# Kernel tuning notes

Hardware: AMD Instinct MI355X
Metric: run time of the kernel (lower is better)

## Reference

```python
import jax, jax.numpy as jnp
import numpy as np

B, S, HID = 1, 2048, 4096
H, HKV, D = 32, 8, 128
GROUPS = H // HKV
ROPE_BASE = 10000.0


def setup_inputs() -> dict:
    key = jax.random.key(0)
    k1, k2, k3, k4, k5 = jax.random.split(key, 5)
    s = 0.02
    return {
        "hidden_states": jax.random.normal(k1, (B, S, HID), dtype=jnp.float32),
        "Wq": jax.random.normal(k2, (H * D, HID), dtype=jnp.float32) * s,
        "Wk": jax.random.normal(k3, (HKV * D, HID), dtype=jnp.float32) * s,
        "Wv": jax.random.normal(k4, (HKV * D, HID), dtype=jnp.float32) * s,
        "Wo": jax.random.normal(k5, (HID, H * D), dtype=jnp.float32) * s,
    }


def _rotate_half(x):
    x1, x2 = x[..., : D // 2], x[..., D // 2 :]
    return jnp.concatenate((-x2, x1), axis=-1)


def _rope_tables(seq_len):
    inv_freq = 1.0 / (ROPE_BASE ** (jnp.arange(0, D, 2, dtype=jnp.float32) / D))
    t = jnp.arange(seq_len, dtype=jnp.float32)
    freqs = jnp.outer(t, inv_freq)            # [S, D/2]
    emb = jnp.concatenate((freqs, freqs), -1)  # [S, D]
    return jnp.cos(emb)[None, None], jnp.sin(emb)[None, None]  # [1,1,S,D]


def reference(hidden_states, Wq, Wk, Wv, Wo):
    b, s, _ = hidden_states.shape
    scale = D ** -0.5
    q = (hidden_states @ Wq.T).reshape(b, s, H, D).transpose(0, 2, 1, 3)    # [B,H,S,D]
    k = (hidden_states @ Wk.T).reshape(b, s, HKV, D).transpose(0, 2, 1, 3)  # [B,HKV,S,D]
    v = (hidden_states @ Wv.T).reshape(b, s, HKV, D).transpose(0, 2, 1, 3)

    cos, sin = _rope_tables(s)
    q = q * cos + _rotate_half(q) * sin
    k = k * cos + _rotate_half(k) * sin

    # repeat_kv: h = kv_h * groups + g -> consecutive repeat along head axis
    k_rep = jnp.repeat(k, GROUPS, axis=1)  # [B,H,S,D]
    v_rep = jnp.repeat(v, GROUPS, axis=1)

    scores = jnp.einsum("bhqd,bhkd->bhqk", q, k_rep) * scale
    causal = jnp.tril(jnp.ones((s, s), dtype=bool))
    scores = jnp.where(causal[None, None], scores, jnp.finfo(scores.dtype).min)
    probs = jax.nn.softmax(scores, axis=-1)
    attn = jnp.einsum("bhqk,bhkd->bhqd", probs, v_rep)  # [B,H,S,D]
    attn = attn.transpose(0, 2, 1, 3).reshape(b, s, H * D)
    return attn @ Wo.T
```

## Files before the change

kernel.cpp:

```cpp
#include <hip/hip_runtime.h>

#define AS1 __attribute__((address_space(1)))
#define AS3 __attribute__((address_space(3)))

typedef __bf16 bf16;
typedef __bf16 bf16x8 __attribute__((ext_vector_type(8)));
typedef float f32x4 __attribute__((ext_vector_type(4)));

__device__ __forceinline__ void gld_lds16(const bf16* g, bf16* l) {
    __builtin_amdgcn_global_load_lds((const AS1 void*)g, (AS3 void*)l, 16, 0, 0);
}

__global__ void cvt4_kernel(const float4* __restrict__ in, ushort4* __restrict__ out, int n4) {
    const int i = blockIdx.x * 256 + threadIdx.x;
    if (i >= n4) return;
    const float4 v = in[i];
    ushort4 r;
    r.x = __builtin_bit_cast(unsigned short, (bf16)v.x);
    r.y = __builtin_bit_cast(unsigned short, (bf16)v.y);
    r.z = __builtin_bit_cast(unsigned short, (bf16)v.z);
    r.w = __builtin_bit_cast(unsigned short, (bf16)v.w);
    out[i] = r;
}

template <int BN, bool OUTF32>
__launch_bounds__(512, 2)
__global__ void gemm8p_kernel(const bf16* __restrict__ A, const bf16* __restrict__ W,
                              void* __restrict__ Cout, int M, int N, int K) {
    constexpr int NF = BN / 64;
    constexpr int IB = BN / 128;
    __shared__ __align__(16) bf16 Asl[4][128 * 32];
    __shared__ __align__(16) bf16 Bsl[4][BN * 32];

    const int tn = blockIdx.x * BN;
    const int tm = blockIdx.y * 128;
    const int tid = threadIdx.x;
    const int wave = tid >> 6;
    const int lane = tid & 63;
    const int laneR = lane & 15;
    const int laneS = lane >> 4;
    const int wmB = (wave >> 2) * 64;
    const int wnB = (wave & 3) * (BN / 4);
    const int NT = K >> 5;

    auto stage = [&](int t) {
        const int slot = t & 3;
        const int k0 = t << 5;
        {
            const int row = tid >> 2, g = tid & 3;
            gld_lds16(A + (size_t)(tm + row) * K + k0 + g * 8, &Asl[slot][wave * 512]);
        }
#pragma unroll
        for (int i = 0; i < IB; ++i) {
            const int row = i * 128 + (tid >> 2), g = tid & 3;
            gld_lds16(W + (size_t)(tn + row) * K + k0 + g * 8,
                      &Bsl[slot][i * 4096 + wave * 512]);
        }
    };

    f32x4 acc[4][NF] = {};

    stage(0); stage(1); stage(2);
    if constexpr (BN == 384) asm volatile("s_waitcnt vmcnt(8)" ::: "memory");
    else                     asm volatile("s_waitcnt vmcnt(6)" ::: "memory");
    __builtin_amdgcn_sched_barrier(0);
    __builtin_amdgcn_s_barrier();
    __builtin_amdgcn_sched_barrier(0);

    for (int t = 0; t < NT; ++t) {
        const int slot = t & 3;
        bf16x8 af[4], bfr[NF];
#pragma unroll
        for (int mf = 0; mf < 4; ++mf)
            af[mf] = *(const bf16x8*)&Asl[slot][(wmB + mf * 16 + laneR) * 32 + laneS * 8];
#pragma unroll
        for (int nf = 0; nf < NF; ++nf)
            bfr[nf] = *(const bf16x8*)&Bsl[slot][(wnB + nf * 16 + laneR) * 32 + laneS * 8];

        if (t + 3 < NT) stage(t + 3);

#pragma unroll
        for (int mf = 0; mf < 4; ++mf)
#pragma unroll
            for (int nf = 0; nf < NF; ++nf)
                acc[mf][nf] = __builtin_amdgcn_mfma_f32_16x16x32_bf16(af[mf], bfr[nf], acc[mf][nf], 0, 0, 0);

        __builtin_amdgcn_sched_barrier(0);
        if (t + 3 < NT) {
            if constexpr (BN == 384) asm volatile("s_waitcnt vmcnt(8)" ::: "memory");
            else                     asm volatile("s_waitcnt vmcnt(6)" ::: "memory");
        } else if (t + 3 == NT) {
            if constexpr (BN == 384) asm volatile("s_waitcnt vmcnt(4)" ::: "memory");
            else                     asm volatile("s_waitcnt vmcnt(3)" ::: "memory");
        } else {
            asm volatile("s_waitcnt vmcnt(0)" ::: "memory");
        }
        __builtin_amdgcn_sched_barrier(0);
        __builtin_amdgcn_s_barrier();
        __builtin_amdgcn_sched_barrier(0);
    }

    const int rbase = laneS * 4;
#pragma unroll
    for (int mf = 0; mf < 4; ++mf)
#pragma unroll
        for (int nf = 0; nf < NF; ++nf)
#pragma unroll
            for (int rr = 0; rr < 4; ++rr) {
                const size_t row = (size_t)tm + wmB + mf * 16 + rbase + rr;
                const size_t col = (size_t)tn + wnB + nf * 16 + laneR;
                if constexpr (OUTF32) ((float*)Cout)[row * N + col] = acc[mf][nf][rr];
                else                  ((bf16*)Cout)[row * N + col] = (bf16)acc[mf][nf][rr];
            }
    (void)M;
}

__global__ void rope_qk_kernel(const bf16* __restrict__ C, bf16* __restrict__ Qr, bf16* __restrict__ Kr) {
    const int idx = blockIdx.x * 256 + threadIdx.x;
    const int NQ = 2048 * 32 * 64;
    const float QSC = 0.12751743561884394f;
    const float LN1E4_64 = 0.14391156831212787f;
    if (idx < NQ) {
        const int f = idx & 63;
        const int t = idx >> 6;
        const int h = t & 31;
        const int s = t >> 5;
        const float x1 = (float)C[(size_t)s * 6144 + h * 128 + f];
        const float x2 = (float)C[(size_t)s * 6144 + h * 128 + f + 64];
        const float th = s * expf(-LN1E4_64 * (float)f);
        const float cs = cosf(th), sn = sinf(th);
        bf16* dst = Qr + ((size_t)h * 2048 + s) * 128 + f;
        dst[0]  = (bf16)((x1 * cs - x2 * sn) * QSC);
        dst[64] = (bf16)((x2 * cs + x1 * sn) * QSC);
    } else {
        const int i2 = idx - NQ;
        const int f = i2 & 63;
        const int t = i2 >> 6;
        const int h = t & 7;
        const int s = t >> 3;
        const float x1 = (float)C[(size_t)s * 6144 + 4096 + h * 128 + f];
        const float x2 = (float)C[(size_t)s * 6144 + 4096 + h * 128 + f + 64];
        const float th = s * expf(-LN1E4_64 * (float)f);
        const float cs = cosf(th), sn = sinf(th);
        bf16* dst = Kr + ((size_t)h * 2048 + s) * 128 + f;
        dst[0]  = (bf16)(x1 * cs - x2 * sn);
        dst[64] = (bf16)(x2 * cs + x1 * sn);
    }
}

__global__ void transpose_v_kernel(const bf16* __restrict__ C, bf16* __restrict__ Vt) {
    __shared__ __align__(16) unsigned short t[64][136];
    const int hkv = blockIdx.x >> 5;
    const int st = blockIdx.x & 31;
    const int s0 = st * 64;
    const int tid = threadIdx.x;
#pragma unroll
    for (int it = 0; it < 4; ++it) {
        const int l = it * 2048 + tid * 8;
        const int r = l >> 7, c = l & 127;
        *(bf16x8*)&t[r][c] = *(const bf16x8*)&C[(size_t)(s0 + r) * 6144 + 5120 + hkv * 128 + c];
    }
    __syncthreads();
#pragma unroll
    for (int it = 0; it < 8; ++it) {
        const int o = it * 1024 + tid * 4;
        const int d = o >> 6, j = o & 63;
        ushort4 pk;
        pk.x = t[j + 0][d];
        pk.y = t[j + 1][d];
        pk.z = t[j + 2][d];
        pk.w = t[j + 3][d];
        *(ushort4*)&Vt[((size_t)hkv * 128 + d) * 2048 + s0 + j] = pk;
    }
}

__launch_bounds__(256, 1)
__global__ void flash_attn_kernel(const bf16* __restrict__ Qr, const bf16* __restrict__ Kr,
                                  const bf16* __restrict__ Vt, bf16* __restrict__ Aout) {
    __shared__ __align__(16) bf16 Klds[2][128 * 128];
    __shared__ __align__(16) bf16 Vlds[2][128 * 128];
    __shared__ __align__(16) char Plds[4][4096];

    const int bid = blockIdx.x;
    const int hkv = bid & 7;
    const int r = bid >> 3;
    const int h = hkv * 4 + (r & 3);
    const int pa = r >> 2;
    const int qbA = 15 - pa, qbB = pa;
    const int tid = threadIdx.x;
    const int wave = tid >> 6, lane = tid & 63;
    const int laneR = lane & 15;
    const int laneS = lane >> 4;
    const int laneK = laneS * 8;
    const int rbase = laneS * 4;

    const bf16* Kh = Kr + (size_t)hkv * 2048 * 128;
    const bf16* Vh = Vt + (size_t)hkv * 128 * 2048;
    char* Pw = Plds[wave];

    auto stageK = [&](int kv0, int buf) {
#pragma unroll
        for (int s = 0; s < 8; ++s) {
            const int chunk = wave * 8 + s;
            const int L = chunk * 64 + lane;
            const int row = L >> 4, sl = L & 15;
            gld_lds16(Kh + (size_t)(kv0 + row) * 128 + ((sl ^ (row & 7)) << 3),
                      &Klds[buf][chunk * 512]);
        }
    };
    auto stageV = [&](int kv0, int buf) {
#pragma unroll
        for (int s = 0; s < 8; ++s) {
            const int chunk = wave * 8 + s;
            const int L = chunk * 64 + lane;
            const int row = L >> 4, sl = L & 15;
            gld_lds16(Vh + (size_t)row * 2048 + kv0 + ((sl ^ (row & 7)) << 3),
                      &Vlds[buf][chunk * 512]);
        }
    };

    int qbcur = qbA;
    int q0w = qbA * 128 + wave * 32;
    int tloc = 0;

    bf16x8 qf[2][4];
    auto loadQ = [&]() {
#pragma unroll
        for (int mi = 0; mi < 2; ++mi)
#pragma unroll
            for (int kc = 0; kc < 4; ++kc)
                qf[mi][kc] = *(const bf16x8*)&Qr[((size_t)h * 2048 + q0w + mi * 16 + laneR) * 128 + kc * 32 + laneK];
    };
    loadQ();

    f32x4 o[2][8] = {};
    float mrow[2][4], lrow[2][4];
#pragma unroll
    for (int mi = 0; mi < 2; ++mi)
#pragma unroll
        for (int rr = 0; rr < 4; ++rr) { mrow[mi][rr] = -1e30f; lrow[mi][rr] = 0.f; }

    stageK(0, 0);
    stageV(0, 0);
    __syncthreads();

    for (int g = 0; g < 17; ++g) {
        const int buf = g & 1;
        if (g < 16) {
            const int tn = (g + 1 <= qbA) ? (g + 1) : (g - qbA);
            stageK(tn * 128, buf ^ 1);
            stageV(tn * 128, buf ^ 1);
        }
        const int kv0 = tloc * 128;

        f32x4 sc[2][8] = {};
        __builtin_amdgcn_s_setprio(1);
#pragma unroll
        for (int kc = 0; kc < 4; ++kc) {
            bf16x8 kf[8];
#pragma unroll
            for (int j = 0; j < 8; ++j) {
                const int row = j * 16 + laneR;
                kf[j] = *(const bf16x8*)((const char*)Klds[buf] + row * 256 +
                                         ((kc * 64 + laneS * 16) ^ ((row & 7) << 4)));
            }
#pragma unroll
            for (int mi = 0; mi < 2; ++mi)
#pragma unroll
                for (int j = 0; j < 8; ++j)
                    sc[mi][j] = __builtin_amdgcn_mfma_f32_16x16x32_bf16(qf[mi][kc], kf[j], sc[mi][j], 0, 0, 0);
        }
        __builtin_amdgcn_s_setprio(0);

        if (tloc == qbcur) {
#pragma unroll
            for (int mi = 0; mi < 2; ++mi)
#pragma unroll
                for (int j = 0; j < 8; ++j)
#pragma unroll
                    for (int rr = 0; rr < 4; ++rr) {
                        const int qr = q0w + mi * 16 + rbase + rr;
                        const int kr = kv0 + j * 16 + laneR;
                        if (kr > qr) sc[mi][j][rr] = -1e30f;
                    }
        }

#pragma unroll
        for (int mi = 0; mi < 2; ++mi) {
#pragma unroll
            for (int rr = 0; rr < 4; ++rr) {
                float v = sc[mi][0][rr];
#pragma unroll
                for (int j = 1; j < 8; ++j) v = fmaxf(v, sc[mi][j][rr]);
                v = fmaxf(v, __shfl_xor(v, 1, 64));
                v = fmaxf(v, __shfl_xor(v, 2, 64));
                v = fmaxf(v, __shfl_xor(v, 4, 64));
                v = fmaxf(v, __shfl_xor(v, 8, 64));
                float m0 = mrow[mi][rr];
                if (v - m0 > 8.0f) {
                    const float fac = __builtin_exp2f(m0 - v);
                    mrow[mi][rr] = v;
                    m0 = v;
                    lrow[mi][rr] *= fac;
#pragma unroll
                    for (int j = 0; j < 8; ++j) o[mi][j][rr] *= fac;
                }
                float rs = 0.f;
#pragma unroll
                for (int j = 0; j < 8; ++j) {
                    const float p = __builtin_exp2f(sc[mi][j][rr] - m0);
                    sc[mi][j][rr] = p;
                    rs += p;
                }
                rs += __shfl_xor(rs, 1, 64);
                rs += __shfl_xor(rs, 2, 64);
                rs += __shfl_xor(rs, 4, 64);
                rs += __shfl_xor(rs, 8, 64);
                lrow[mi][rr] += rs;
            }
        }

#pragma unroll
        for (int hf = 0; hf < 2; ++hf) {
#pragma unroll
            for (int mi = 0; mi < 2; ++mi)
#pragma unroll
                for (int j = 0; j < 4; ++j)
#pragma unroll
                    for (int rr = 0; rr < 4; ++rr) {
                        const int row = mi * 16 + rbase + rr;
                        *(bf16*)(Pw + row * 128 + ((j * 32 + laneR * 2) ^ ((row & 7) << 4))) =
                            (bf16)sc[mi][hf * 4 + j][rr];
                    }
            __builtin_amdgcn_s_setprio(1);
#pragma unroll
            for (int kc = 0; kc < 2; ++kc) {
                bf16x8 pf[2];
#pragma unroll
                for (int mi = 0; mi < 2; ++mi) {
                    const int row = mi * 16 + laneR;
                    pf[mi] = *(const bf16x8*)(Pw + row * 128 + ((kc * 64 + laneS * 16) ^ ((row & 7) << 4)));
                }
                const int kcg = hf * 2 + kc;
                bf16x8 vf[8];
#pragma unroll
                for (int j = 0; j < 8; ++j) {
                    const int row = j * 16 + laneR;
                    vf[j] = *(const bf16x8*)((const char*)Vlds[buf] + row * 256 +
                                             ((kcg * 64 + laneS * 16) ^ ((row & 7) << 4)));
                }
#pragma unroll
                for (int mi = 0; mi < 2; ++mi)
#pragma unroll
                    for (int j = 0; j < 8; ++j)
                        o[mi][j] = __builtin_amdgcn_mfma_f32_16x16x32_bf16(pf[mi], vf[j], o[mi][j], 0, 0, 0);
            }
            __builtin_amdgcn_s_setprio(0);
        }

        if (tloc == qbcur) {
#pragma unroll
            for (int mi = 0; mi < 2; ++mi) {
                float rinv[4];
#pragma unroll
                for (int rr = 0; rr < 4; ++rr) rinv[rr] = 1.0f / lrow[mi][rr];
#pragma unroll
                for (int j = 0; j < 8; ++j)
#pragma unroll
                    for (int rr = 0; rr < 4; ++rr) {
                        const size_t row = (size_t)q0w + mi * 16 + rbase + rr;
                        Aout[row * 4096 + h * 128 + j * 16 + laneR] = (bf16)(o[mi][j][rr] * rinv[rr]);
                    }
            }
            if (g < 16) {
                qbcur = qbB;
                q0w = qbB * 128 + wave * 32;
                tloc = 0;
                loadQ();
#pragma unroll
                for (int mi = 0; mi < 2; ++mi)
#pragma unroll
                    for (int rr = 0; rr < 4; ++rr) { mrow[mi][rr] = -1e30f; lrow[mi][rr] = 0.f; }
#pragma unroll
                for (int mi = 0; mi < 2; ++mi)
#pragma unroll
                    for (int j = 0; j < 8; ++j)
                        o[mi][j] = f32x4{0.f, 0.f, 0.f, 0.f};
            }
        } else {
            ++tloc;
        }

        __syncthreads();
    }
}

extern "C" void kernel_launch(void* const* d_in, const int* in_sizes, int n_in,
                              void* d_out, int out_size, void* d_ws, size_t ws_size,
                              hipStream_t stream) {
    const float* hidden = (const float*)d_in[0];
    const float* Wq = (const float*)d_in[1];
    const float* Wk = (const float*)d_in[2];
    const float* Wv = (const float*)d_in[3];
    const float* Wo = (const float*)d_in[4];
    float* out = (float*)d_out;
    char* ws = (char*)d_ws;

    bf16* hs = (bf16*)(ws + 0);
    bf16* Wb = (bf16*)(ws + 16777216);
    bf16* Cq = (bf16*)(ws + 100663296);
    bf16* Qr = (bf16*)(ws + 125829120);
    bf16* Kr = (bf16*)(ws + 142606336);
    bf16* Vt = (bf16*)(ws + 146800640);
    bf16* At = (bf16*)(ws + 150994944);
    (void)ws_size; (void)in_sizes; (void)n_in; (void)out_size;

    cvt4_kernel<<<8192, 256, 0, stream>>>((const float4*)hidden, (ushort4*)hs, 2097152);
    cvt4_kernel<<<16384, 256, 0, stream>>>((const float4*)Wq, (ushort4*)(Wb + 0), 4194304);
    cvt4_kernel<<<4096, 256, 0, stream>>>((const float4*)Wk, (ushort4*)(Wb + 16777216), 1048576);
    cvt4_kernel<<<4096, 256, 0, stream>>>((const float4*)Wv, (ushort4*)(Wb + 20971520), 1048576);
    cvt4_kernel<<<16384, 256, 0, stream>>>((const float4*)Wo, (ushort4*)(Wb + 25165824), 4194304);

    gemm8p_kernel<384, false><<<dim3(16, 16), 512, 0, stream>>>(hs, Wb, Cq, 2048, 6144, 4096);

    rope_qk_kernel<<<20480, 256, 0, stream>>>(Cq, Qr, Kr);

    transpose_v_kernel<<<256, 256, 0, stream>>>(Cq, Vt);

    flash_attn_kernel<<<256, 256, 0, stream>>>(Qr, Kr, Vt, At);

    gemm8p_kernel<256, true><<<dim3(16, 16), 512, 0, stream>>>(At, Wb + 25165824, out, 2048, 4096, 4096);
}
```

Measured before the change: 353.0 us.

## Replace GEMM with 4-wave 128x256 tile kernel using swizzled LDS ring

Replaces the 8-wave, 4-slot GEMM with a 256-thread kernel. Each wave owns a 128x64 output slice, and the kernel uses a 3-slot LDS ring with prefetch distance 2. LDS is XOR-swizzled to avoid bank conflicts on the fragment reads, and the MFMA block is wrapped in s_setprio. This gives each wave more MFMA work per LDS read and fixes the tile shape at 128x256 for both projections, which changes the QKV grid to 24x16. The trade-offs are higher register pressure from 32 accumulators per wave and a shallower prefetch pipeline.

```diff
diff --git a/kernel.cpp b/kernel.cpp
--- a/kernel.cpp
+++ b/kernel.cpp
@@ -23,78 +23,76 @@
     out[i] = r;
 }
 
-template <int BN, bool OUTF32>
-__launch_bounds__(512, 2)
-__global__ void gemm8p_kernel(const bf16* __restrict__ A, const bf16* __restrict__ W,
-                              void* __restrict__ Cout, int M, int N, int K) {
-    constexpr int NF = BN / 64;
-    constexpr int IB = BN / 128;
-    __shared__ __align__(16) bf16 Asl[4][128 * 32];
-    __shared__ __align__(16) bf16 Bsl[4][BN * 32];
-
-    const int tn = blockIdx.x * BN;
+template <bool OUTF32>
+__launch_bounds__(256, 2)
+__global__ void gemm_ring_kernel(const bf16* __restrict__ A, const bf16* __restrict__ W,
+                                 void* __restrict__ Cout, int M, int N, int K) {
+    __shared__ __align__(16) bf16 Asl[3][128 * 32];
+    __shared__ __align__(16) bf16 Bsl[3][256 * 32];
+
+    const int tn = blockIdx.x * 256;
     const int tm = blockIdx.y * 128;
     const int tid = threadIdx.x;
     const int wave = tid >> 6;
     const int lane = tid & 63;
     const int laneR = lane & 15;
     const int laneS = lane >> 4;
-    const int wmB = (wave >> 2) * 64;
-    const int wnB = (wave & 3) * (BN / 4);
+    const int wnB = wave * 64;
     const int NT = K >> 5;
+    const int sofs = (laneS ^ ((laneR >> 1) & 3)) << 3;
 
     auto stage = [&](int t) {
-        const int slot = t & 3;
+        const int slot = t % 3;
         const int k0 = t << 5;
-        {
-            const int row = tid >> 2, g = tid & 3;
-            gld_lds16(A + (size_t)(tm + row) * K + k0 + g * 8, &Asl[slot][wave * 512]);
-        }
-#pragma unroll
-        for (int i = 0; i < IB; ++i) {
-            const int row = i * 128 + (tid >> 2), g = tid & 3;
-            gld_lds16(W + (size_t)(tn + row) * K + k0 + g * 8,
-                      &Bsl[slot][i * 4096 + wave * 512]);
+#pragma unroll
+        for (int iss = 0; iss < 2; ++iss) {
+            const int c = iss * 256 + wave * 64 + lane;
+            const int row = c >> 2;
+            const int sg = (c & 3) ^ ((row >> 1) & 3);
+            gld_lds16(A + (size_t)(tm + row) * K + k0 + sg * 8,
+                      &Asl[slot][iss * 2048 + wave * 512]);
+        }
+#pragma unroll
+        for (int iss = 0; iss < 4; ++iss) {
+            const int c = iss * 256 + wave * 64 + lane;
+            const int row = c >> 2;
+            const int sg = (c & 3) ^ ((row >> 1) & 3);
+            gld_lds16(W + (size_t)(tn + row) * K + k0 + sg * 8,
+                      &Bsl[slot][iss * 2048 + wave * 512]);
         }
     };
 
-    f32x4 acc[4][NF] = {};
-
-    stage(0); stage(1); stage(2);
-    if constexpr (BN == 384) asm volatile("s_waitcnt vmcnt(8)" ::: "memory");
-    else                     asm volatile("s_waitcnt vmcnt(6)" ::: "memory");
+    f32x4 acc[8][4] = {};
+
+    stage(0); stage(1);
+    asm volatile("s_waitcnt vmcnt(6)" ::: "memory");
     __builtin_amdgcn_sched_barrier(0);
     __builtin_amdgcn_s_barrier();
     __builtin_amdgcn_sched_barrier(0);
 
     for (int t = 0; t < NT; ++t) {
-        const int slot = t & 3;
-        bf16x8 af[4], bfr[NF];
-#pragma unroll
-        for (int mf = 0; mf < 4; ++mf)
-            af[mf] = *(const bf16x8*)&Asl[slot][(wmB + mf * 16 + laneR) * 32 + laneS * 8];
-#pragma unroll
-        for (int nf = 0; nf < NF; ++nf)
-            bfr[nf] = *(const bf16x8*)&Bsl[slot][(wnB + nf * 16 + laneR) * 32 + laneS * 8];
-
-        if (t + 3 < NT) stage(t + 3);
-
-#pragma unroll
-        for (int mf = 0; mf < 4; ++mf)
-#pragma unroll
-            for (int nf = 0; nf < NF; ++nf)
+        const int slot = t % 3;
+        if (t + 2 < NT) stage(t + 2);
+
+        bf16x8 af[8], bfr[4];
+#pragma unroll
+        for (int nf = 0; nf < 4; ++nf)
+            bfr[nf] = *(const bf16x8*)&Bsl[slot][(wnB + nf * 16 + laneR) * 32 + sofs];
+#pragma unroll
+        for (int mf = 0; mf < 8; ++mf)
+            af[mf] = *(const bf16x8*)&Asl[slot][(mf * 16 + laneR) * 32 + sofs];
+
+        __builtin_amdgcn_s_setprio(1);
+#pragma unroll
+        for (int mf = 0; mf < 8; ++mf)
+#pragma unroll
+            for (int nf = 0; nf < 4; ++nf)
                 acc[mf][nf] = __builtin_amdgcn_mfma_f32_16x16x32_bf16(af[mf], bfr[nf], acc[mf][nf], 0, 0, 0);
+        __builtin_amdgcn_s_setprio(0);
 
         __builtin_amdgcn_sched_barrier(0);
-        if (t + 3 < NT) {
-            if constexpr (BN == 384) asm volatile("s_waitcnt vmcnt(8)" ::: "memory");
-            else                     asm volatile("s_waitcnt vmcnt(6)" ::: "memory");
-        } else if (t + 3 == NT) {
-            if constexpr (BN == 384) asm volatile("s_waitcnt vmcnt(4)" ::: "memory");
-            else                     asm volatile("s_waitcnt vmcnt(3)" ::: "memory");
-        } else {
-            asm volatile("s_waitcnt vmcnt(0)" ::: "memory");
-        }
+        if (t + 2 < NT) asm volatile("s_waitcnt vmcnt(6)" ::: "memory");
+        else            asm volatile("s_waitcnt vmcnt(0)" ::: "memory");
         __builtin_amdgcn_sched_barrier(0);
         __builtin_amdgcn_s_barrier();
         __builtin_amdgcn_sched_barrier(0);
@@ -102,12 +100,12 @@
 
     const int rbase = laneS * 4;
 #pragma unroll
-    for (int mf = 0; mf < 4; ++mf)
-#pragma unroll
-        for (int nf = 0; nf < NF; ++nf)
+    for (int mf = 0; mf < 8; ++mf)
+#pragma unroll
+        for (int nf = 0; nf < 4; ++nf)
 #pragma unroll
             for (int rr = 0; rr < 4; ++rr) {
-                const size_t row = (size_t)tm + wmB + mf * 16 + rbase + rr;
+                const size_t row = (size_t)tm + mf * 16 + rbase + rr;
                 const size_t col = (size_t)tn + wnB + nf * 16 + laneR;
                 if constexpr (OUTF32) ((float*)Cout)[row * N + col] = acc[mf][nf][rr];
                 else                  ((bf16*)Cout)[row * N + col] = (bf16)acc[mf][nf][rr];
@@ -421,7 +419,7 @@
     cvt4_kernel<<<4096, 256, 0, stream>>>((const float4*)Wv, (ushort4*)(Wb + 20971520), 1048576);
     cvt4_kernel<<<16384, 256, 0, stream>>>((const float4*)Wo, (ushort4*)(Wb + 25165824), 4194304);
 
-    gemm8p_kernel<384, false><<<dim3(16, 16), 512, 0, stream>>>(hs, Wb, Cq, 2048, 6144, 4096);
+    gemm_ring_kernel<false><<<dim3(24, 16), 256, 0, stream>>>(hs, Wb, Cq, 2048, 6144, 4096);
 
     rope_qk_kernel<<<20480, 256, 0, stream>>>(Cq, Qr, Kr);
 
@@ -429,5 +427,5 @@
 
     flash_attn_kernel<<<256, 256, 0, stream>>>(Qr, Kr, Vt, At);
 
-    gemm8p_kernel<256, true><<<dim3(16, 16), 512, 0, stream>>>(At, Wb + 25165824, out, 2048, 4096, 4096);
-}
+    gemm_ring_kernel<true><<<dim3(16, 16), 256, 0, stream>>>(At, Wb + 25165824, out, 2048, 4096, 4096);
+}
```

Result: slower. 440.8 us (+24.9%).

## Add 256x256-tile eight-phase GEMM with swizzled LDS for QKV projection

Applied to the files above, without the earlier changes.

Adds a new GEMM kernel for the QKV projection that uses 256x256 output tiles with a 64-wide K step and double-buffered LDS. It uses an XOR swizzle on LDS slots to avoid bank conflicts and interleaves quarter-tile loads with MFMA phases separated by barriers, raising MFMA priority through setprio. Larger tiles raise arithmetic intensity and cut redundant global traffic. In exchange the grid drops to 192 blocks, fewer than the CU count, and the extra barriers add synchronisation cost. The older gemm kernel is simplified to assume BN=256, which is now its only remaining use.

```diff
diff --git a/kernel.cpp b/kernel.cpp
--- a/kernel.cpp
+++ b/kernel.cpp
@@ -10,6 +10,9 @@
 __device__ __forceinline__ void gld_lds16(const bf16* g, bf16* l) {
     __builtin_amdgcn_global_load_lds((const AS1 void*)g, (AS3 void*)l, 16, 0, 0);
 }
+
+#define SB0 __builtin_amdgcn_sched_barrier(0)
+#define BARX do { SB0; __builtin_amdgcn_s_barrier(); SB0; } while (0)
 
 __global__ void cvt4_kernel(const float4* __restrict__ in, ushort4* __restrict__ out, int n4) {
     const int i = blockIdx.x * 256 + threadIdx.x;
@@ -23,6 +26,121 @@
     out[i] = r;
 }
 
+template <bool OUTF32>
+__launch_bounds__(512, 2)
+__global__ void gemm_8ph_kernel(const bf16* __restrict__ A, const bf16* __restrict__ W,
+                                void* __restrict__ Cout, int M, int N, int K) {
+    __shared__ __align__(16) bf16 Asl[2][256 * 64];
+    __shared__ __align__(16) bf16 Bsl[2][256 * 64];
+
+    const int tn = blockIdx.x * 256;
+    const int tm = blockIdx.y * 256;
+    const int tid = threadIdx.x;
+    const int wave = tid >> 6;
+    const int lane = tid & 63;
+    const int laneR = lane & 15;
+    const int laneS = lane >> 4;
+    const int wmB = (wave >> 2) * 128;
+    const int wnB = (wave & 3) * 64;
+    const int NT = K >> 6;
+    const int NI = NT >> 1;
+
+    auto stageA = [&](int t, int h) {
+        if (t >= NT) return;
+        const int d = t & 1, k0 = t << 6;
+#pragma unroll
+        for (int iss = 0; iss < 2; ++iss) {
+            const int c = iss * 512 + tid;
+            const int row = c >> 3, sl = c & 7;
+            gld_lds16(A + (size_t)(tm + h * 128 + row) * K + k0 + ((sl ^ (row & 7)) << 3),
+                      &Asl[d][h * 8192 + (iss * 512 + wave * 64) * 8]);
+        }
+    };
+    auto stageB = [&](int t, int h) {
+        if (t >= NT) return;
+        const int d = t & 1, k0 = t << 6;
+#pragma unroll
+        for (int iss = 0; iss < 2; ++iss) {
+            const int c = iss * 512 + tid;
+            const int row = c >> 3, sl = c & 7;
+            gld_lds16(W + (size_t)(tn + h * 128 + row) * K + k0 + ((sl ^ (row & 7)) << 3),
+                      &Bsl[d][h * 8192 + (iss * 512 + wave * 64) * 8]);
+        }
+    };
+
+    bf16x8 aF[8], bF0[4], bF1[4];
+    f32x4 acc[8][4] = {};
+
+#define RD_A(d, mh) do { _Pragma("unroll") for (int m = 0; m < 4; ++m) \
+    _Pragma("unroll") for (int ks = 0; ks < 2; ++ks) { \
+        const int row_ = wmB + (mh) * 64 + m * 16 + laneR; \
+        const int sl_ = (ks * 4 + laneS) ^ (row_ & 7); \
+        aF[m * 2 + ks] = *(const bf16x8*)&Asl[d][row_ * 64 + sl_ * 8]; } } while (0)
+
+#define RD_B(d, nh, DST) do { _Pragma("unroll") for (int n = 0; n < 2; ++n) \
+    _Pragma("unroll") for (int ks = 0; ks < 2; ++ks) { \
+        const int row_ = wnB + (nh) * 32 + n * 16 + laneR; \
+        const int sl_ = (ks * 4 + laneS) ^ (row_ & 7); \
+        DST[n * 2 + ks] = *(const bf16x8*)&Bsl[d][row_ * 64 + sl_ * 8]; } } while (0)
+
+#define MMAQ(mh, nh, BSRC) do { __builtin_amdgcn_s_setprio(1); \
+    _Pragma("unroll") for (int m = 0; m < 4; ++m) \
+    _Pragma("unroll") for (int n = 0; n < 2; ++n) \
+    _Pragma("unroll") for (int ks = 0; ks < 2; ++ks) \
+        acc[(mh) * 4 + m][(nh) * 2 + n] = __builtin_amdgcn_mfma_f32_16x16x32_bf16( \
+            aF[m * 2 + ks], BSRC[n * 2 + ks], acc[(mh) * 4 + m][(nh) * 2 + n], 0, 0, 0); \
+    __builtin_amdgcn_s_setprio(0); } while (0)
+
+    stageA(0, 0); stageA(0, 1); stageB(0, 0); stageB(0, 1); stageA(1, 0);
+    SB0; asm volatile("s_waitcnt vmcnt(2)" ::: "memory"); BARX;
+
+    for (int i = 0; i < NI; ++i) {
+        const int u = i * 2;
+        const bool last = (i == NI - 1);
+        RD_A(0, 0); RD_B(0, 0, bF0); stageA(u + 1, 1);
+        BARX; MMAQ(0, 0, bF0); BARX;
+        RD_B(0, 1, bF1); stageB(u + 1, 0);
+        BARX; MMAQ(0, 1, bF1); BARX;
+        RD_A(0, 1); stageB(u + 1, 1);
+        BARX; MMAQ(1, 1, bF1); BARX;
+        RD_B(0, 0, bF0); stageA(u + 2, 0);
+        BARX; MMAQ(1, 0, bF0);
+        SB0;
+        if (last) asm volatile("s_waitcnt vmcnt(0)" ::: "memory");
+        else      asm volatile("s_waitcnt vmcnt(2)" ::: "memory");
+        BARX;
+        RD_A(1, 0); RD_B(1, 0, bF0); stageA(u + 2, 1);
+        BARX; MMAQ(0, 0, bF0); BARX;
+        RD_B(1, 1, bF1); stageB(u + 2, 0);
+        BARX; MMAQ(0, 1, bF1); BARX;
+        RD_A(1, 1); stageB(u + 2, 1);
+        BARX; MMAQ(1, 1, bF1); BARX;
+        RD_B(1, 0, bF0); stageA(u + 3, 0);
+        BARX; MMAQ(1, 0, bF0);
+        SB0;
+        if (last) asm volatile("s_waitcnt vmcnt(0)" ::: "memory");
+        else      asm volatile("s_waitcnt vmcnt(2)" ::: "memory");
+        BARX;
+    }
+#undef RD_A
+#undef RD_B
+#undef MMAQ
+
+    const int rbase = laneS * 4;
+#pragma unroll
+    for (int mf = 0; mf < 8; ++mf)
+#pragma unroll
+        for (int nf = 0; nf < 4; ++nf)
+#pragma unroll
+            for (int rr = 0; rr < 4; ++rr) {
+                const size_t row = (size_t)tm + wmB + mf * 16 + rbase + rr;
+                const size_t col = (size_t)tn + wnB + nf * 16 + laneR;
+                if constexpr (OUTF32) ((float*)Cout)[row * N + col] = acc[mf][nf][rr];
+                else                  ((bf16*)Cout)[row * N + col] = (bf16)acc[mf][nf][rr];
+            }
+    (void)M;
+}
+
 template <int BN, bool OUTF32>
 __launch_bounds__(512, 2)
 __global__ void gemm8p_kernel(const bf16* __restrict__ A, const bf16* __restrict__ W,
@@ -61,11 +179,10 @@
     f32x4 acc[4][NF] = {};
 
     stage(0); stage(1); stage(2);
-    if constexpr (BN == 384) asm volatile("s_waitcnt vmcnt(8)" ::: "memory");
-    else                     asm volatile("s_waitcnt vmcnt(6)" ::: "memory");
-    __builtin_amdgcn_sched_barrier(0);
+    asm volatile("s_waitcnt vmcnt(6)" ::: "memory");
+    SB0;
     __builtin_amdgcn_s_barrier();
-    __builtin_amdgcn_sched_barrier(0);
+    SB0;
 
     for (int t = 0; t < NT; ++t) {
         const int slot = t & 3;
@@ -85,19 +202,13 @@
             for (int nf = 0; nf < NF; ++nf)
                 acc[mf][nf] = __builtin_amdgcn_mfma_f32_16x16x32_bf16(af[mf], bfr[nf], acc[mf][nf], 0, 0, 0);
 
-        __builtin_amdgcn_sched_barrier(0);
-        if (t + 3 < NT) {
-            if constexpr (BN == 384) asm volatile("s_waitcnt vmcnt(8)" ::: "memory");
-            else                     asm volatile("s_waitcnt vmcnt(6)" ::: "memory");
-        } else if (t + 3 == NT) {
-            if constexpr (BN == 384) asm volatile("s_waitcnt vmcnt(4)" ::: "memory");
-            else                     asm volatile("s_waitcnt vmcnt(3)" ::: "memory");
-        } else {
-            asm volatile("s_waitcnt vmcnt(0)" ::: "memory");
-        }
-        __builtin_amdgcn_sched_barrier(0);
+        SB0;
+        if (t + 3 < NT)      asm volatile("s_waitcnt vmcnt(6)" ::: "memory");
+        else if (t + 3 == NT) asm volatile("s_waitcnt vmcnt(3)" ::: "memory");
+        else                  asm volatile("s_waitcnt vmcnt(0)" ::: "memory");
+        SB0;
         __builtin_amdgcn_s_barrier();
-        __builtin_amdgcn_sched_barrier(0);
+        SB0;
     }
 
     const int rbase = laneS * 4;
@@ -421,7 +532,7 @@
     cvt4_kernel<<<4096, 256, 0, stream>>>((const float4*)Wv, (ushort4*)(Wb + 20971520), 1048576);
     cvt4_kernel<<<16384, 256, 0, stream>>>((const float4*)Wo, (ushort4*)(Wb + 25165824), 4194304);
 
-    gemm8p_kernel<384, false><<<dim3(16, 16), 512, 0, stream>>>(hs, Wb, Cq, 2048, 6144, 4096);
+    gemm_8ph_kernel<false><<<dim3(24, 8), 512, 0, stream>>>(hs, Wb, Cq, 2048, 6144, 4096);
 
     rope_qk_kernel<<<20480, 256, 0, stream>>>(Cq, Qr, Kr);
 
```

New measurement: 363.1 us. 1.03x slower.
